# Kernel optimization log

Hardware: AMD Instinct MI355X
Metric: run time of the kernel (lower is better)

## Reference

```python
import jax, jax.numpy as jnp
import numpy as np

N = 1024      # num_waves
L = 32        # latent_dim
H = 64        # hidden_dim
EPS = 1e-6
SELF_SCALE = 0.5
INT_SCALE = 0.3


def _xavier(k, shape, gain=0.5):
    fan_out, fan_in = shape
    std = gain * np.sqrt(2.0 / (fan_in + fan_out))
    return (jax.random.normal(k, shape, jnp.float32) * std).astype(jnp.float32)


def setup_inputs() -> dict:
    key = jax.random.key(0)
    ks = jax.random.split(key, 12)
    d = {}
    d['state'] = jax.random.normal(ks[0], (N * (L + 1),), jnp.float32)
    # SelfDynamicsNetwork: L->H->H->L, tanh, xavier_normal gain=0.5, zero bias
    d['Ws1'] = _xavier(ks[1], (H, L)); d['bs1'] = jnp.zeros((H,), jnp.float32)
    d['Ws2'] = _xavier(ks[2], (H, H)); d['bs2'] = jnp.zeros((H,), jnp.float32)
    d['Ws3'] = _xavier(ks[3], (L, H)); d['bs3'] = jnp.zeros((L,), jnp.float32)
    # InteractionNetwork: 4L->H->H->L
    d['Wi1'] = _xavier(ks[4], (H, 4 * L)); d['bi1'] = jnp.zeros((H,), jnp.float32)
    d['Wi2'] = _xavier(ks[5], (H, H));     d['bi2'] = jnp.zeros((H,), jnp.float32)
    d['Wi3'] = _xavier(ks[6], (L, H));     d['bi3'] = jnp.zeros((L,), jnp.float32)
    # QuantumPhaseMixer
    d['phase_w'] = jax.random.normal(ks[7], (L,), jnp.float32) * 0.1
    d['Wc'] = _xavier(ks[8], (L, 2 * L), gain=1.0)
    d['bc'] = jnp.zeros((L,), jnp.float32)
    # per-wave aggressiveness
    d['aggr'] = jnp.ones((N,), jnp.float32) * 0.5
    return d


def reference(state, Ws1, bs1, Ws2, bs2, Ws3, bs3,
              Wi1, bi1, Wi2, bi2, Wi3, bi3,
              phase_w, Wc, bc, aggr):
    s = state.reshape(N, L + 1)
    h = s[:, :L]          # [N, L]
    phases = s[:, L]      # [N]

    def mlp(x, W1, b1, W2, b2, W3, b3):
        x = jnp.tanh(x @ W1.T + b1)
        x = jnp.tanh(x @ W2.T + b2)
        return x @ W3.T + b3

    self_term = mlp(h, Ws1, bs1, Ws2, bs2, Ws3, bs3)   # [N, L]
    dh = self_term  # prev_state is None -> estimated velocity = self_dynamics(h)

    # pairwise distance factor
    diff = h[:, None, :] - h[None, :, :]                # [N, N, L] (h_i - h_j)
    dist = jnp.linalg.norm(diff, axis=-1) + EPS         # [N, N]
    dfac = jnp.minimum(1.0 / dist, 2.0)

    # InteractionNetwork on concat([h_i, h_j, dh_i, dh_j]): split first layer
    a_i = h @ Wi1[:, :L].T + dh @ Wi1[:, 2 * L:3 * L].T           # [N, H]
    b_j = h @ Wi1[:, L:2 * L].T + dh @ Wi1[:, 3 * L:].T + bi1    # [N, H]
    x1 = jnp.tanh(a_i[:, None, :] + b_j[None, :, :])              # [N, N, H]
    x2 = jnp.tanh(x1 @ Wi2.T + bi2)                               # [N, N, H]
    k_ij = x2 @ Wi3.T + bi3                                       # [N, N, L]

    # QuantumPhaseMixer
    phase_diff = phases[:, None] - phases[None, :]                # [N, N]
    pf = jnp.cos(phase_diff[..., None] * phase_w)                 # [N, N, L]
    coh = jax.nn.sigmoid((h @ Wc[:, :L].T)[:, None, :]
                         + (h @ Wc[:, L:].T)[None, :, :] + bc)    # [N, N, L]
    quantum = pf * coh * (-diff)                                  # h_j - h_i = -diff

    agg = jax.nn.sigmoid(aggr)                                    # [N]
    inter = dfac[..., None] * k_ij * agg[:, None, None] + quantum # [N, N, L]
    mask = 1.0 - jnp.eye(N, dtype=inter.dtype)                    # skip j == i
    isum = jnp.einsum('ijl,ij->il', inter, mask)                  # sum over j

    # env is None -> speed_mults = 1, refractions = 0
    dh_dt = SELF_SCALE * self_term + INT_SCALE * isum
    dphase = 0.1 + 0.05 * jnp.sum(jnp.abs(isum), axis=-1)
    return jnp.concatenate([dh_dt, dphase[:, None]], axis=1).reshape(-1)
```

## Files before the change

### kernel.cpp

```cpp
#include <hip/hip_runtime.h>
#include <hip/hip_bf16.h>
#include <math.h>

#define NN 1024
#define LDIM 32
#define HDIM 64

#define WS_SELF 0
#define WS_AA   (WS_SELF + NN*LDIM)
#define WS_CI   (WS_AA   + NN*HDIM)
#define WS_AGG  (WS_CI   + NN*LDIM)
#define WS_BI2  (WS_AGG  + NN)
#define WS_BI3  (WS_BI2  + HDIM)
#define WS_BCB  (WS_BI3  + LDIM)
#define WS_FEND (WS_BCB  + LDIM)

#define U_BJB  0
#define U_HJB  (U_BJB + NN*HDIM)
#define U_JT   (U_HJB + NN*LDIM)
#define U_W2B  (U_JT  + NN*LDIM*4)
#define U_W3B  (U_W2B + HDIM*HDIM)
#define U_END  (U_W3B + LDIM*HDIM)

#define PK_W1  0
#define PK_W2  1024
#define PK_W3  3072
#define PK_WI1 4096
#define PK_WC  8192
#define PK_END 9216

typedef __attribute__((ext_vector_type(8))) short bf16x8;
typedef __attribute__((ext_vector_type(4))) float f32x4;

__device__ __forceinline__ float fast_rcp(float x) { return __builtin_amdgcn_rcpf(x); }
__device__ __forceinline__ float fast_tanh(float x) {
    float e = __builtin_amdgcn_exp2f(x * 2.88539008f);
    return 1.0f - 2.0f * fast_rcp(e + 1.0f);
}
__device__ __forceinline__ float fast_sigmoid(float x) {
    return fast_rcp(1.0f + __builtin_amdgcn_exp2f(x * -1.44269504f));
}
__device__ __forceinline__ float blo(unsigned int u) { union { unsigned int i; float f; } v; v.i = u << 16; return v.f; }
__device__ __forceinline__ float bhi(unsigned int u) { union { unsigned int i; float f; } v; v.i = u & 0xffff0000u; return v.f; }
__device__ __forceinline__ float bf2f(unsigned short u) { union { unsigned int i; float f; } v; v.i = ((unsigned int)u) << 16; return v.f; }
__device__ __forceinline__ unsigned short f2bf(float f) {
    __hip_bfloat16 b = __float2bfloat16(f);
    unsigned short u; __builtin_memcpy(&u, &b, 2); return u;
}
__device__ __forceinline__ unsigned int pk2(float a, float b) {
    float2 t; t.x = a; t.y = b;
    __hip_bfloat162 h = __float22bfloat162_rn(t);
    unsigned int u; __builtin_memcpy(&u, &h, 4); return u;
}

__global__ __launch_bounds__(256) void precompute(
    const float* __restrict__ state,
    const float* __restrict__ Ws1, const float* __restrict__ bs1,
    const float* __restrict__ Ws2, const float* __restrict__ bs2,
    const float* __restrict__ Ws3, const float* __restrict__ bs3,
    const float* __restrict__ Wi1, const float* __restrict__ bi1,
    const float* __restrict__ Wi2, const float* __restrict__ bi2,
    const float* __restrict__ Wi3, const float* __restrict__ bi3,
    const float* __restrict__ phw, const float* __restrict__ Wc,
    const float* __restrict__ bc,  const float* __restrict__ aggr,
    float* __restrict__ ws, unsigned short* __restrict__ wsu) {
    const int tid = threadIdx.x;
    const int w = tid >> 6, t = tid & 63;
    const int i = blockIdx.x * 4 + w;

    __shared__ unsigned int wlds[PK_END];
    __shared__ float shh[4][32], shdh[4][32], sht1[4][64], sht2[4][64];
    __shared__ float shph[4];

    {
        const float2* s1 = (const float2*)Ws1;
        #pragma unroll
        for (int r = 0; r < 4; r++) { int e = tid + r * 256; int f = e >> 4, k2 = e & 15;
            float2 v = s1[e]; wlds[PK_W1 + k2 * 64 + f] = pk2(v.x, v.y); }
        const float2* s2 = (const float2*)Ws2;
        #pragma unroll
        for (int r = 0; r < 8; r++) { int e = tid + r * 256; int f = e >> 5, k2 = e & 31;
            float2 v = s2[e]; wlds[PK_W2 + k2 * 64 + f] = pk2(v.x, v.y); }
        const float2* s3 = (const float2*)Ws3;
        #pragma unroll
        for (int r = 0; r < 4; r++) { int e = tid + r * 256; int f = e >> 5, k2 = e & 31;
            float2 v = s3[e]; wlds[PK_W3 + k2 * 32 + f] = pk2(v.x, v.y); }
        const float2* si = (const float2*)Wi1;
        #pragma unroll
        for (int r = 0; r < 16; r++) { int e = tid + r * 256; int f = e >> 6, c2 = e & 63;
            float2 v = si[e]; wlds[PK_WI1 + c2 * 64 + f] = pk2(v.x, v.y); }
        const float2* sc = (const float2*)Wc;
        #pragma unroll
        for (int r = 0; r < 4; r++) { int e = tid + r * 256; int f = e >> 5, c2 = e & 31;
            float2 v = sc[e]; wlds[PK_WC + c2 * 32 + f] = pk2(v.x, v.y); }
    }
    if (blockIdx.x == 0) {
        #pragma unroll
        for (int r = 0; r < 16; r++) { int e = tid + r * 256; wsu[U_W2B + e] = f2bf(Wi2[e]); }
        #pragma unroll
        for (int r = 0; r < 8; r++)  { int e = tid + r * 256; wsu[U_W3B + e] = f2bf(Wi3[e]); }
        if (tid < HDIM) ws[WS_BI2 + tid] = bi2[tid];
        if (tid < LDIM) { ws[WS_BI3 + tid] = bi3[tid]; ws[WS_BCB + tid] = bc[tid]; }
    }

    float sv = (t < 33) ? state[i * 33 + t] : 0.f;
    if (t < 32) shh[w][t] = sv;
    if (t == 32) shph[w] = sv;
    if (t == 33) ws[WS_AGG + i] = fast_sigmoid(aggr[i]);
    __syncthreads();

    {
        float s = bs1[t];
        const unsigned int* W = wlds + PK_W1;
        #pragma unroll
        for (int k2 = 0; k2 < 16; k2++) {
            unsigned int p = W[k2 * 64 + t];
            s = fmaf(blo(p), shh[w][2 * k2], s);
            s = fmaf(bhi(p), shh[w][2 * k2 + 1], s);
        }
        sht1[w][t] = fast_tanh(s);
    }
    __syncthreads();
    {
        float s = bs2[t];
        const unsigned int* W = wlds + PK_W2;
        #pragma unroll
        for (int k2 = 0; k2 < 32; k2++) {
            unsigned int p = W[k2 * 64 + t];
            s = fmaf(blo(p), sht1[w][2 * k2], s);
            s = fmaf(bhi(p), sht1[w][2 * k2 + 1], s);
        }
        sht2[w][t] = fast_tanh(s);
    }
    __syncthreads();
    if (t < 32) {
        float s = bs3[t];
        const unsigned int* W = wlds + PK_W3;
        #pragma unroll
        for (int k2 = 0; k2 < 32; k2++) {
            unsigned int p = W[k2 * 32 + t];
            s = fmaf(blo(p), sht2[w][2 * k2], s);
            s = fmaf(bhi(p), sht2[w][2 * k2 + 1], s);
        }
        ws[WS_SELF + i * 32 + t] = s;
        shdh[w][t] = s;
    }
    __syncthreads();
    {
        float sa = 0.f, sb = bi1[t];
        const unsigned int* W = wlds + PK_WI1;
        #pragma unroll
        for (int k2 = 0; k2 < 16; k2++) {
            float h0 = shh[w][2 * k2], h1 = shh[w][2 * k2 + 1];
            float d0 = shdh[w][2 * k2], d1 = shdh[w][2 * k2 + 1];
            unsigned int wa  = W[k2 * 64 + t];
            unsigned int wb  = W[(16 + k2) * 64 + t];
            unsigned int wa2 = W[(32 + k2) * 64 + t];
            unsigned int wb2 = W[(48 + k2) * 64 + t];
            sa = fmaf(blo(wa), h0, sa);  sa = fmaf(bhi(wa), h1, sa);
            sb = fmaf(blo(wb), h0, sb);  sb = fmaf(bhi(wb), h1, sb);
            sa = fmaf(blo(wa2), d0, sa); sa = fmaf(bhi(wa2), d1, sa);
            sb = fmaf(blo(wb2), d0, sb); sb = fmaf(bhi(wb2), d1, sb);
        }
        ws[WS_AA + i * 64 + t] = sa;
        wsu[U_BJB + i * 64 + t] = f2bf(sb);
    }
    if (t < 32) {
        float si = 0.f, sj = 0.f;
        const unsigned int* W = wlds + PK_WC;
        #pragma unroll
        for (int m2 = 0; m2 < 16; m2++) {
            float h0 = shh[w][2 * m2], h1 = shh[w][2 * m2 + 1];
            unsigned int wi = W[m2 * 32 + t];
            unsigned int wj = W[(16 + m2) * 32 + t];
            si = fmaf(blo(wi), h0, si); si = fmaf(bhi(wi), h1, si);
            sj = fmaf(blo(wj), h0, sj); sj = fmaf(bhi(wj), h1, sj);
        }
        ws[WS_CI + i * 32 + t] = si;
        float h = shh[w][t];
        wsu[U_HJB + i * 32 + t] = f2bf(h);
        float sc, cc;
        __sincosf(shph[w] * phw[t], &sc, &cc);
        uint2 jt; jt.x = pk2(h, sj); jt.y = pk2(cc, sc);
        *(uint2*)(wsu + U_JT + (i * 32 + t) * 4) = jt;
    }
}

__global__ __launch_bounds__(256) void pair_kernel(
    const float* __restrict__ ws, const unsigned short* __restrict__ wsu,
    float* __restrict__ out) {
    const int i    = blockIdx.x;
    const int tid  = threadIdx.x;
    const int w    = tid >> 6;
    const int lane = tid & 63;
    const int q    = lane >> 4;
    const int m    = lane & 15;
    const int jw   = w * 16;
    const int sub  = lane & 3;

    __shared__ unsigned short W2ls[64 * 72];
    __shared__ unsigned short W3ls[32 * 72];
    __shared__ unsigned short x2ls[4 * 16 * 72];
    __shared__ float aLS[64];
    __shared__ float redT[4][32], redU[4][32], redV[4][32];
    __shared__ float sfw[4];

    if (tid < 64) aLS[tid] = ws[WS_AA + i * 64 + tid];
    {
        int row = tid >> 2, c = (tid & 3) * 16;
        const uint4* s2 = (const uint4*)(wsu + U_W2B + row * 64 + c);
        uint4 d0 = s2[0], d1 = s2[1];
        uint4* dd = (uint4*)(&W2ls[row * 72 + c]);
        dd[0] = d0; dd[1] = d1;
        if (row < 32) {
            const uint4* s3 = (const uint4*)(wsu + U_W3B + row * 64 + c);
            uint4 e0 = s3[0], e1 = s3[1];
            uint4* d3 = (uint4*)(&W3ls[row * 72 + c]);
            d3[0] = e0; d3[1] = e1;
        }
    }
    float hi8[8];
    {
        uint4 hv4 = *(const uint4*)(wsu + U_HJB + i * 32 + sub * 8);
        unsigned int hd[4] = {hv4.x, hv4.y, hv4.z, hv4.w};
        #pragma unroll
        for (int e = 0; e < 4; e++) { hi8[2 * e] = blo(hd[e]); hi8[2 * e + 1] = bhi(hd[e]); }
    }
    f32x4 b2q[4];
    #pragma unroll
    for (int nb = 0; nb < 4; nb++) {
        float4 bv = *(const float4*)(ws + WS_BI2 + nb * 16 + q * 4);
        b2q[nb][0] = bv.x; b2q[nb][1] = bv.y; b2q[nb][2] = bv.z; b2q[nb][3] = bv.w;
    }
    float hiv[2], cibv[2];
    #pragma unroll
    for (int lb = 0; lb < 2; lb++) {
        int l = lb * 16 + m;
        hiv[lb]  = bf2f(wsu[U_HJB + i * 32 + l]);
        cibv[lb] = ws[WS_CI + i * 32 + l] + ws[WS_BCB + l];
    }
    const float aggi = ws[WS_AGG + i];
    const float sub0 = (sub == 0) ? 1.0f : 0.0f;

    const unsigned short* hp = wsu + U_HJB + (jw + (lane >> 2)) * 32 + sub * 8;
    const unsigned short* bp = wsu + U_BJB + (jw + m) * 64 + q * 8;
    const unsigned short* jp = wsu + U_JT + ((jw + q * 4) * 32 + m) * 4;

    uint4 hvA = *(const uint4*)hp;
    uint4 b0A = *(const uint4*)bp;
    uint4 b1A = *(const uint4*)(bp + 32);
    uint4 hvB, b0B, b1B;
    __syncthreads();

    f32x4 accK[2];
    #pragma unroll
    for (int lb = 0; lb < 2; lb++) { accK[lb][0]=0.f; accK[lb][1]=0.f; accK[lb][2]=0.f; accK[lb][3]=0.f; }
    float aU[2] = {0.f, 0.f}, aV[2] = {0.f, 0.f};
    float sumfac = 0.f;

    unsigned short* xw = &x2ls[w * 16 * 72];

    auto body = [&](int T, uint4 hvc, uint4 b0c, uint4 b1c,
                    uint4& hvn, uint4& b0n, uint4& b1n) {
        hp += 2048; bp += 4096;
        hvn = *(const uint4*)hp;
        b0n = *(const uint4*)bp;
        b1n = *(const uint4*)(bp + 32);
        uint2 jt[8];
        #pragma unroll
        for (int r = 0; r < 4; r++) {
            jt[r]     = *(const uint2*)(jp + r * 128);
            jt[4 + r] = *(const uint2*)(jp + 64 + r * 128);
        }
        jp += 8192;

        float facm;
        {
            unsigned int hd[4] = {hvc.x, hvc.y, hvc.z, hvc.w};
            float s = 0.f;
            #pragma unroll
            for (int e = 0; e < 4; e++) {
                float d0 = hi8[2 * e]     - blo(hd[e]);
                float d1 = hi8[2 * e + 1] - bhi(hd[e]);
                s = fmaf(d0, d0, s); s = fmaf(d1, d1, s);
            }
            s += __shfl_xor(s, 1); s += __shfl_xor(s, 2);
            int jj = T * 64 + jw + (lane >> 2);
            float facown = fminf(fast_rcp(sqrtf(s) + 1e-6f), 2.0f) * aggi;
            facown = (jj == i) ? 0.0f : facown;
            sumfac = fmaf(sub0, facown, sumfac);
            facm = __shfl(facown, 4 * m);
        }

        bf16x8 afr[2];
        {
            unsigned int bd[8] = {b0c.x, b0c.y, b0c.z, b0c.w, b1c.x, b1c.y, b1c.z, b1c.w};
            #pragma unroll
            for (int s = 0; s < 2; s++) {
                union { uint4 u4; bf16x8 v; } pkd;
                #pragma unroll
                for (int e = 0; e < 4; e++) {
                    const float* ab = &aLS[s * 32 + q * 8 + 2 * e];
                    float x0 = fast_tanh(ab[0] + blo(bd[s * 4 + e]));
                    float x1 = fast_tanh(ab[1] + bhi(bd[s * 4 + e]));
                    ((unsigned int*)&pkd.u4)[e] = pk2(x0, x1);
                }
                afr[s] = pkd.v;
            }
        }

        f32x4 accA[4];
        #pragma unroll
        for (int nb = 0; nb < 4; nb++) {
            f32x4 acc = b2q[nb];
            #pragma unroll
            for (int s = 0; s < 2; s++) {
                bf16x8 w2f = *(const bf16x8*)(&W2ls[(nb * 16 + m) * 72 + s * 32 + q * 8]);
                acc = __builtin_amdgcn_mfma_f32_16x16x32_bf16(w2f, afr[s], acc, 0, 0, 0);
            }
            accA[nb] = acc;
        }
        #pragma unroll
        for (int nb = 0; nb < 4; nb++) {
            float t0 = fast_tanh(accA[nb][0]) * facm;
            float t1 = fast_tanh(accA[nb][1]) * facm;
            float t2 = fast_tanh(accA[nb][2]) * facm;
            float t3 = fast_tanh(accA[nb][3]) * facm;
            uint2 pk; pk.x = pk2(t0, t1); pk.y = pk2(t2, t3);
            *(uint2*)(&xw[m * 72 + nb * 16 + q * 4]) = pk;
        }

        {
            bf16x8 x2f[2];
            #pragma unroll
            for (int s = 0; s < 2; s++)
                x2f[s] = *(const bf16x8*)(&xw[m * 72 + s * 32 + q * 8]);
            #pragma unroll
            for (int lb = 0; lb < 2; lb++) {
                #pragma unroll
                for (int s = 0; s < 2; s++) {
                    bf16x8 w3f = *(const bf16x8*)(&W3ls[(lb * 16 + m) * 72 + s * 32 + q * 8]);
                    accK[lb] = __builtin_amdgcn_mfma_f32_16x16x32_bf16(x2f[s], w3f, accK[lb], 0, 0, 0);
                }
            }
        }

        #pragma unroll
        for (int lb = 0; lb < 2; lb++) {
            float u = 0.f, v = 0.f;
            #pragma unroll
            for (int r = 0; r < 4; r++) {
                uint2 jv = jt[lb * 4 + r];
                float hj = blo(jv.x), cj = bhi(jv.x);
                float pjc = blo(jv.y), pjs = bhi(jv.y);
                float coh = fast_sigmoid(cibv[lb] + cj);
                float cd  = coh * (hiv[lb] - hj);
                u = fmaf(cd, pjc, u);
                v = fmaf(cd, pjs, v);
            }
            aU[lb] += u; aV[lb] += v;
        }
    };

    #pragma unroll 1
    for (int T = 0; T < 16; T += 2) {
        body(T,     hvA, b0A, b1A, hvB, b0B, b1B);
        body(T + 1, hvB, b0B, b1B, hvA, b0A, b1A);
    }

    float T1[2];
    #pragma unroll
    for (int lb = 0; lb < 2; lb++) {
        T1[lb] = (accK[lb][0] + accK[lb][1]) + (accK[lb][2] + accK[lb][3]);
        T1[lb] += __shfl_xor(T1[lb], 16); T1[lb] += __shfl_xor(T1[lb], 32);
        aU[lb] += __shfl_xor(aU[lb], 16); aU[lb] += __shfl_xor(aU[lb], 32);
        aV[lb] += __shfl_xor(aV[lb], 16); aV[lb] += __shfl_xor(aV[lb], 32);
    }
    sumfac += __shfl_xor(sumfac, 1);  sumfac += __shfl_xor(sumfac, 2);
    sumfac += __shfl_xor(sumfac, 4);  sumfac += __shfl_xor(sumfac, 8);
    sumfac += __shfl_xor(sumfac, 16); sumfac += __shfl_xor(sumfac, 32);
    if (lane < 16) {
        redT[w][m] = T1[0];      redT[w][16 + m] = T1[1];
        redU[w][m] = aU[0];      redU[w][16 + m] = aU[1];
        redV[w][m] = aV[0];      redV[w][16 + m] = aV[1];
    }
    if (lane == 0) sfw[w] = sumfac;
    __syncthreads();
    if (tid < 32) {
        int l = tid;
        float t1 = (redT[0][l] + redT[1][l]) + (redT[2][l] + redT[3][l]);
        float uu = (redU[0][l] + redU[1][l]) + (redU[2][l] + redU[3][l]);
        float vv = (redV[0][l] + redV[1][l]) + (redV[2][l] + redV[3][l]);
        float sf = (sfw[0] + sfw[1]) + (sfw[2] + sfw[3]);
        uint2 jti = *(const uint2*)(wsu + U_JT + (i * 32 + l) * 4);
        float pic = blo(jti.y), pis = bhi(jti.y);
        float isum = t1 + sf * ws[WS_BI3 + l] - (pic * uu + pis * vv);
        out[i * 33 + l] = 0.5f * ws[WS_SELF + i * 32 + l] + 0.3f * isum;
        redT[0][l] = fabsf(isum);
    }
    __syncthreads();
    if (tid == 0) {
        float s = 0.f;
        #pragma unroll
        for (int l = 0; l < 32; l++) s += redT[0][l];
        out[i * 33 + 32] = 0.1f + 0.05f * s;
    }
}

extern "C" void kernel_launch(void* const* d_in, const int* in_sizes, int n_in,
                              void* d_out, int out_size, void* d_ws, size_t ws_size,
                              hipStream_t stream) {
    const float* state   = (const float*)d_in[0];
    const float* Ws1     = (const float*)d_in[1];
    const float* bs1     = (const float*)d_in[2];
    const float* Ws2     = (const float*)d_in[3];
    const float* bs2     = (const float*)d_in[4];
    const float* Ws3     = (const float*)d_in[5];
    const float* bs3     = (const float*)d_in[6];
    const float* Wi1     = (const float*)d_in[7];
    const float* bi1     = (const float*)d_in[8];
    const float* Wi2     = (const float*)d_in[9];
    const float* bi2     = (const float*)d_in[10];
    const float* Wi3     = (const float*)d_in[11];
    const float* bi3     = (const float*)d_in[12];
    const float* phase_w = (const float*)d_in[13];
    const float* Wc      = (const float*)d_in[14];
    const float* bc      = (const float*)d_in[15];
    const float* aggr    = (const float*)d_in[16];

    float* ws = (float*)d_ws;
    unsigned short* wsu = (unsigned short*)(ws + WS_FEND);
    float* out = (float*)d_out;

    precompute<<<256, 256, 0, stream>>>(state, Ws1, bs1, Ws2, bs2, Ws3, bs3,
                                        Wi1, bi1, Wi2, bi2, Wi3, bi3,
                                        phase_w, Wc, bc, aggr, ws, wsu);
    pair_kernel<<<NN, 256, 0, stream>>>(ws, wsu, out);
}
```

Measured before the change: 154.6 us.

## Double-buffer x2 tile to overlap layer-3 MFMA with next tile; prescale exponents

The x2 staging buffer in LDS is double-buffered, so the layer-3 MFMA for the previous tile runs after the next tile's loads and distance work, with a final drain after the loop. That overlaps the LDS write/read round trip with other work. The log2(e) scale factors for tanh and sigmoid are folded into the weights, biases and precomputed activations, removing multiplies from the inner loop. The tanh*fac product is rewritten as a single fma, and the distance reciprocal uses rsq, which drops the epsilon. The cost is twice the x2 LDS footprint and slightly changed numerics from bf16 rounding of the prescaled values.

```diff
diff --git a/kernel.cpp b/kernel.cpp
--- a/kernel.cpp
+++ b/kernel.cpp
@@ -12,8 +12,7 @@
 #define WS_AGG  (WS_CI   + NN*LDIM)
 #define WS_BI2  (WS_AGG  + NN)
 #define WS_BI3  (WS_BI2  + HDIM)
-#define WS_BCB  (WS_BI3  + LDIM)
-#define WS_FEND (WS_BCB  + LDIM)
+#define WS_FEND (WS_BI3  + LDIM)
 
 #define U_BJB  0
 #define U_HJB  (U_BJB + NN*HDIM)
@@ -29,16 +28,22 @@
 #define PK_WC  8192
 #define PK_END 9216
 
+#define K2P  2.88539008f
+#define K1N  (-1.44269504f)
+
 typedef __attribute__((ext_vector_type(8))) short bf16x8;
 typedef __attribute__((ext_vector_type(4))) float f32x4;
 
 __device__ __forceinline__ float fast_rcp(float x) { return __builtin_amdgcn_rcpf(x); }
 __device__ __forceinline__ float fast_tanh(float x) {
-    float e = __builtin_amdgcn_exp2f(x * 2.88539008f);
+    float e = __builtin_amdgcn_exp2f(x * K2P);
     return 1.0f - 2.0f * fast_rcp(e + 1.0f);
 }
+__device__ __forceinline__ float tanh_pre(float xp) {
+    return 1.0f - 2.0f * fast_rcp(__builtin_amdgcn_exp2f(xp) + 1.0f);
+}
 __device__ __forceinline__ float fast_sigmoid(float x) {
-    return fast_rcp(1.0f + __builtin_amdgcn_exp2f(x * -1.44269504f));
+    return fast_rcp(1.0f + __builtin_amdgcn_exp2f(x * K1N));
 }
 __device__ __forceinline__ float blo(unsigned int u) { union { unsigned int i; float f; } v; v.i = u << 16; return v.f; }
 __device__ __forceinline__ float bhi(unsigned int u) { union { unsigned int i; float f; } v; v.i = u & 0xffff0000u; return v.f; }
@@ -96,11 +101,11 @@
     }
     if (blockIdx.x == 0) {
         #pragma unroll
-        for (int r = 0; r < 16; r++) { int e = tid + r * 256; wsu[U_W2B + e] = f2bf(Wi2[e]); }
+        for (int r = 0; r < 16; r++) { int e = tid + r * 256; wsu[U_W2B + e] = f2bf(Wi2[e] * K2P); }
         #pragma unroll
         for (int r = 0; r < 8; r++)  { int e = tid + r * 256; wsu[U_W3B + e] = f2bf(Wi3[e]); }
-        if (tid < HDIM) ws[WS_BI2 + tid] = bi2[tid];
-        if (tid < LDIM) { ws[WS_BI3 + tid] = bi3[tid]; ws[WS_BCB + tid] = bc[tid]; }
+        if (tid < HDIM) ws[WS_BI2 + tid] = bi2[tid] * K2P;
+        if (tid < LDIM) ws[WS_BI3 + tid] = bi3[tid];
     }
 
     float sv = (t < 33) ? state[i * 33 + t] : 0.f;
@@ -162,8 +167,8 @@
             sa = fmaf(blo(wa2), d0, sa); sa = fmaf(bhi(wa2), d1, sa);
             sb = fmaf(blo(wb2), d0, sb); sb = fmaf(bhi(wb2), d1, sb);
         }
-        ws[WS_AA + i * 64 + t] = sa;
-        wsu[U_BJB + i * 64 + t] = f2bf(sb);
+        ws[WS_AA + i * 64 + t]  = sa * K2P;
+        wsu[U_BJB + i * 64 + t] = f2bf(sb * K2P);
     }
     if (t < 32) {
         float si = 0.f, sj = 0.f;
@@ -176,12 +181,12 @@
             si = fmaf(blo(wi), h0, si); si = fmaf(bhi(wi), h1, si);
             sj = fmaf(blo(wj), h0, sj); sj = fmaf(bhi(wj), h1, sj);
         }
-        ws[WS_CI + i * 32 + t] = si;
+        ws[WS_CI + i * 32 + t] = (si + bc[t]) * K1N;
         float h = shh[w][t];
         wsu[U_HJB + i * 32 + t] = f2bf(h);
         float sc, cc;
         __sincosf(shph[w] * phw[t], &sc, &cc);
-        uint2 jt; jt.x = pk2(h, sj); jt.y = pk2(cc, sc);
+        uint2 jt; jt.x = pk2(h, sj * K1N); jt.y = pk2(cc, sc);
         *(uint2*)(wsu + U_JT + (i * 32 + t) * 4) = jt;
     }
 }
@@ -200,7 +205,7 @@
 
     __shared__ unsigned short W2ls[64 * 72];
     __shared__ unsigned short W3ls[32 * 72];
-    __shared__ unsigned short x2ls[4 * 16 * 72];
+    __shared__ unsigned short x2ls[4 * 2 * 16 * 72];
     __shared__ float aLS[64];
     __shared__ float redT[4][32], redU[4][32], redV[4][32];
     __shared__ float sfw[4];
@@ -237,7 +242,7 @@
     for (int lb = 0; lb < 2; lb++) {
         int l = lb * 16 + m;
         hiv[lb]  = bf2f(wsu[U_HJB + i * 32 + l]);
-        cibv[lb] = ws[WS_CI + i * 32 + l] + ws[WS_BCB + l];
+        cibv[lb] = ws[WS_CI + i * 32 + l];
     }
     const float aggi = ws[WS_AGG + i];
     const float sub0 = (sub == 0) ? 1.0f : 0.0f;
@@ -258,10 +263,27 @@
     float aU[2] = {0.f, 0.f}, aV[2] = {0.f, 0.f};
     float sumfac = 0.f;
 
-    unsigned short* xw = &x2ls[w * 16 * 72];
+    unsigned short* xb0 = &x2ls[w * 2 * 1152];
+    unsigned short* xb1 = xb0 + 1152;
+
+    auto stageB = [&](const unsigned short* xb) {
+        bf16x8 x2f[2];
+        #pragma unroll
+        for (int s = 0; s < 2; s++)
+            x2f[s] = *(const bf16x8*)(&xb[m * 72 + s * 32 + q * 8]);
+        #pragma unroll
+        for (int lb = 0; lb < 2; lb++) {
+            #pragma unroll
+            for (int s = 0; s < 2; s++) {
+                bf16x8 w3f = *(const bf16x8*)(&W3ls[(lb * 16 + m) * 72 + s * 32 + q * 8]);
+                accK[lb] = __builtin_amdgcn_mfma_f32_16x16x32_bf16(x2f[s], w3f, accK[lb], 0, 0, 0);
+            }
+        }
+    };
 
     auto body = [&](int T, uint4 hvc, uint4 b0c, uint4 b1c,
-                    uint4& hvn, uint4& b0n, uint4& b1n) {
+                    uint4& hvn, uint4& b0n, uint4& b1n,
+                    unsigned short* xcur, const unsigned short* xprev) {
         hp += 2048; bp += 4096;
         hvn = *(const uint4*)hp;
         b0n = *(const uint4*)bp;
@@ -273,6 +295,8 @@
             jt[4 + r] = *(const uint2*)(jp + 64 + r * 128);
         }
         jp += 8192;
+
+        if (T > 0) stageB(xprev);
 
         float facm;
         {
@@ -286,11 +310,12 @@
             }
             s += __shfl_xor(s, 1); s += __shfl_xor(s, 2);
             int jj = T * 64 + jw + (lane >> 2);
-            float facown = fminf(fast_rcp(sqrtf(s) + 1e-6f), 2.0f) * aggi;
+            float facown = fminf(__builtin_amdgcn_rsqf(s), 2.0f) * aggi;
             facown = (jj == i) ? 0.0f : facown;
             sumfac = fmaf(sub0, facown, sumfac);
             facm = __shfl(facown, 4 * m);
         }
+        const float fm2 = -2.0f * facm;
 
         bf16x8 afr[2];
         {
@@ -301,8 +326,8 @@
                 #pragma unroll
                 for (int e = 0; e < 4; e++) {
                     const float* ab = &aLS[s * 32 + q * 8 + 2 * e];
-                    float x0 = fast_tanh(ab[0] + blo(bd[s * 4 + e]));
-                    float x1 = fast_tanh(ab[1] + bhi(bd[s * 4 + e]));
+                    float x0 = tanh_pre(ab[0] + blo(bd[s * 4 + e]));
+                    float x1 = tanh_pre(ab[1] + bhi(bd[s * 4 + e]));
                     ((unsigned int*)&pkd.u4)[e] = pk2(x0, x1);
                 }
                 afr[s] = pkd.v;
@@ -322,27 +347,14 @@
         }
         #pragma unroll
         for (int nb = 0; nb < 4; nb++) {
-            float t0 = fast_tanh(accA[nb][0]) * facm;
-            float t1 = fast_tanh(accA[nb][1]) * facm;
-            float t2 = fast_tanh(accA[nb][2]) * facm;
-            float t3 = fast_tanh(accA[nb][3]) * facm;
+            float r0 = fast_rcp(__builtin_amdgcn_exp2f(accA[nb][0]) + 1.0f);
+            float r1 = fast_rcp(__builtin_amdgcn_exp2f(accA[nb][1]) + 1.0f);
+            float r2 = fast_rcp(__builtin_amdgcn_exp2f(accA[nb][2]) + 1.0f);
+            float r3 = fast_rcp(__builtin_amdgcn_exp2f(accA[nb][3]) + 1.0f);
+            float t0 = fmaf(fm2, r0, facm), t1 = fmaf(fm2, r1, facm);
+            float t2 = fmaf(fm2, r2, facm), t3 = fmaf(fm2, r3, facm);
             uint2 pk; pk.x = pk2(t0, t1); pk.y = pk2(t2, t3);
-            *(uint2*)(&xw[m * 72 + nb * 16 + q * 4]) = pk;
-        }
-
-        {
-            bf16x8 x2f[2];
-            #pragma unroll
-            for (int s = 0; s < 2; s++)
-                x2f[s] = *(const bf16x8*)(&xw[m * 72 + s * 32 + q * 8]);
-            #pragma unroll
-            for (int lb = 0; lb < 2; lb++) {
-                #pragma unroll
-                for (int s = 0; s < 2; s++) {
-                    bf16x8 w3f = *(const bf16x8*)(&W3ls[(lb * 16 + m) * 72 + s * 32 + q * 8]);
-                    accK[lb] = __builtin_amdgcn_mfma_f32_16x16x32_bf16(x2f[s], w3f, accK[lb], 0, 0, 0);
-                }
-            }
+            *(uint2*)(&xcur[m * 72 + nb * 16 + q * 4]) = pk;
         }
 
         #pragma unroll
@@ -353,7 +365,7 @@
                 uint2 jv = jt[lb * 4 + r];
                 float hj = blo(jv.x), cj = bhi(jv.x);
                 float pjc = blo(jv.y), pjs = bhi(jv.y);
-                float coh = fast_sigmoid(cibv[lb] + cj);
+                float coh = fast_rcp(1.0f + __builtin_amdgcn_exp2f(cibv[lb] + cj));
                 float cd  = coh * (hiv[lb] - hj);
                 u = fmaf(cd, pjc, u);
                 v = fmaf(cd, pjs, v);
@@ -364,9 +376,10 @@
 
     #pragma unroll 1
     for (int T = 0; T < 16; T += 2) {
-        body(T,     hvA, b0A, b1A, hvB, b0B, b1B);
-        body(T + 1, hvB, b0B, b1B, hvA, b0A, b1A);
-    }
+        body(T,     hvA, b0A, b1A, hvB, b0B, b1B, xb0, xb1);
+        body(T + 1, hvB, b0B, b1B, hvA, b0A, b1A, xb1, xb0);
+    }
+    stageB(xb1);
 
     float T1[2];
     #pragma unroll
```

After: 150.6 us (median of 2 runs). 1.03x faster.
